# Kernel optimization log

Hardware: AMD Instinct MI355X
Metric: run time of the kernel (lower is better)

The kernel has to match this reference:

```python
import jax, jax.numpy as jnp
import numpy as np

EPS = 1e-5

def _ln(x, w, b):
    mu = jnp.mean(x, -1, keepdims=True)
    var = jnp.mean((x - mu) ** 2, -1, keepdims=True)
    return (x - mu) * jax.lax.rsqrt(var + EPS) * w + b

def setup_inputs() -> dict:
    key = jax.random.key(0)
    ks = jax.random.split(key, 12)
    B, H, W, C = 4, 32, 32, 768
    nh, hd, hidden = 12, 64, 3072
    s = lambda k, sh, fan: jax.random.normal(k, sh, jnp.float32) * (fan ** -0.5)
    return {
        "x": jax.random.normal(ks[0], (B, H, W, C), jnp.float32),
        "norm1_w": jnp.ones((C,), jnp.float32),
        "norm1_b": jnp.zeros((C,), jnp.float32),
        "qkv_w": s(ks[1], (C, 3 * C), C),
        "qkv_b": jnp.zeros((3 * C,), jnp.float32),
        "proj_w": s(ks[2], (C, C), C),
        "proj_b": jnp.zeros((C,), jnp.float32),
        "rel_h": jnp.ones((2 * H - 1, hd), jnp.float32),
        "rel_w": jnp.ones((2 * W - 1, hd), jnp.float32),
        "norm2_w": jnp.ones((C,), jnp.float32),
        "norm2_b": jnp.zeros((C,), jnp.float32),
        "mlp_w1": s(ks[3], (C, hidden), C),
        "mlp_b1": jnp.zeros((hidden,), jnp.float32),
        "mlp_w2": s(ks[4], (hidden, C), hidden),
        "mlp_b2": jnp.zeros((C,), jnp.float32),
    }

def reference(x, norm1_w, norm1_b, qkv_w, qkv_b, proj_w, proj_b, rel_h, rel_w,
              norm2_w, norm2_b, mlp_w1, mlp_b1, mlp_w2, mlp_b2):
    B, H, W, C = x.shape
    nh = 12
    hd = C // nh
    scale = hd ** -0.5
    S = H * W

    xn = _ln(x, norm1_w, norm1_b)
    qkv = (xn.reshape(B, S, C) @ qkv_w + qkv_b)            # [B,S,3C]
    qkv = qkv.reshape(B, S, 3, nh, hd).transpose(2, 0, 3, 1, 4).reshape(3, B * nh, S, hd)
    q, k, v = qkv[0], qkv[1], qkv[2]                        # [B*nh,S,hd]

    attn = jnp.einsum('bqd,bkd->bqk', q * scale, k)         # [B*nh,S,S]

    # relative position bias (q_size == k_size == H or W)
    idx_h = jnp.arange(H)[:, None] - jnp.arange(H)[None, :] + (H - 1)
    idx_w = jnp.arange(W)[:, None] - jnp.arange(W)[None, :] + (W - 1)
    Rh = rel_h[idx_h]                                       # [H,H,hd]
    Rw = rel_w[idx_w]                                       # [W,W,hd]
    q4 = q.reshape(B * nh, H, W, hd)                        # unscaled q, as in source
    bias_h = jnp.einsum('bhwc,hkc->bhwk', q4, Rh)           # [B*nh,H,W,H]
    bias_w = jnp.einsum('bhwc,wkc->bhwk', q4, Rw)           # [B*nh,H,W,W]
    attn = (attn.reshape(B * nh, H, W, H, W)
            + bias_h[:, :, :, :, None]
            + bias_w[:, :, :, None, :]).reshape(B * nh, S, S)

    attn = jax.nn.softmax(attn, axis=-1)
    out = jnp.einsum('bqk,bkd->bqd', attn, v)               # [B*nh,S,hd]
    out = out.reshape(B, nh, H, W, hd).transpose(0, 2, 3, 1, 4).reshape(B, H, W, C)
    x = out @ proj_w + proj_b + x

    xn = _ln(x, norm2_w, norm2_b)
    h = jax.nn.gelu(xn @ mlp_w1 + mlp_b1, approximate=False)
    return h @ mlp_w2 + mlp_b2 + x
```

## Files before the change

### kernel.cpp

```cpp
#include <hip/hip_runtime.h>
#include <hip/hip_bf16.h>
#include <cstdint>
#include <cstddef>

typedef __bf16 bf16x8 __attribute__((ext_vector_type(8)));
typedef float  f32x4  __attribute__((ext_vector_type(4)));
typedef unsigned short u16x8 __attribute__((ext_vector_type(8)));

#define S_TOT 1024
#define NH 12
#define HD 64
#define NBH 48
#define CDIM 768
#define L2E 1.44269504088896f

static __device__ __forceinline__ unsigned short f2bf(float f) {
    unsigned int u = __builtin_bit_cast(unsigned int, f);
    u += 0x7FFFu + ((u >> 16) & 1u);
    return (unsigned short)(u >> 16);
}

static __device__ __forceinline__ float exp2_raw(float x) {
    float r;
    asm("v_exp_f32 %0, %1" : "=v"(r) : "v"(x));
    return r;
}

static __device__ __forceinline__ float gelu_fast(float x) {
    float u = x * (1.0f + 0.044715f * x * x);
    float e = exp2_raw(-2.3022090f * u);
    return x / (1.0f + e);
}

static __device__ __forceinline__ void async16(void* lds, const void* g) {
    __builtin_amdgcn_global_load_lds(
        (const __attribute__((address_space(1))) unsigned int*)g,
        (__attribute__((address_space(3))) unsigned int*)lds, 16, 0, 0);
}

static __device__ __forceinline__ int xcd_swz(int orig, int nwg) {
    return (orig & 7) * (nwg >> 3) + (orig >> 3);
}

__launch_bounds__(256)
__global__ void ln_kernel(const float* __restrict__ x, const float* __restrict__ w,
                          const float* __restrict__ b, unsigned short* __restrict__ out)
{
    const int row = blockIdx.x;
    const int tid = threadIdx.x;
    const float* xr = x + (size_t)row * CDIM;
    float v0 = xr[tid], v1 = xr[tid + 256], v2 = xr[tid + 512];
    float s  = v0 + v1 + v2;
    float s2 = v0 * v0 + v1 * v1 + v2 * v2;
    #pragma unroll
    for (int off = 32; off > 0; off >>= 1) {
        s  += __shfl_xor(s,  off);
        s2 += __shfl_xor(s2, off);
    }
    __shared__ float ss[4], ss2[4];
    const int wid = tid >> 6;
    if ((tid & 63) == 0) { ss[wid] = s; ss2[wid] = s2; }
    __syncthreads();
    s  = ss[0] + ss[1] + ss[2] + ss[3];
    s2 = ss2[0] + ss2[1] + ss2[2] + ss2[3];
    const float mu  = s * (1.0f / CDIM);
    const float var = s2 * (1.0f / CDIM) - mu * mu;
    const float rs  = rsqrtf(var + 1e-5f);
    unsigned short* orow = out + (size_t)row * CDIM;
    float vv[3] = {v0, v1, v2};
    #pragma unroll
    for (int i = 0; i < 3; ++i) {
        int c = tid + i * 256;
        orow[c] = f2bf((vv[i] - mu) * rs * w[c] + b[c]);
    }
}

__launch_bounds__(256)
__global__ void wt_all_kernel(const float* __restrict__ qkv_w, const float* __restrict__ proj_w,
                              const float* __restrict__ w1, const float* __restrict__ w2,
                              unsigned short* __restrict__ wTq, unsigned short* __restrict__ wTp,
                              unsigned short* __restrict__ wT1, unsigned short* __restrict__ wT2)
{
    __shared__ float tile[32][33];
    int id = blockIdx.x;
    const float* W; unsigned short* WT; int K, N, ko, no;
    if (id < 1728)      { W = qkv_w;  WT = wTq; K = 768;  N = 2304;            ko = id % 24; no = id / 24; }
    else if (id < 2304) { W = proj_w; WT = wTp; K = 768;  N = 768;  id -= 1728; ko = id % 24; no = id / 24; }
    else if (id < 4608) { W = w1;     WT = wT1; K = 768;  N = 3072; id -= 2304; ko = id % 24; no = id / 24; }
    else                { W = w2;     WT = wT2; K = 3072; N = 768;  id -= 4608; ko = id % 96; no = id / 96; }
    const int k0 = ko * 32, n0 = no * 32;
    const int tx = threadIdx.x & 31, ty = threadIdx.x >> 5;
    #pragma unroll
    for (int i = 0; i < 4; ++i) {
        int kk = ty + i * 8;
        tile[kk][tx] = W[(size_t)(k0 + kk) * N + n0 + tx];
    }
    __syncthreads();
    #pragma unroll
    for (int i = 0; i < 4; ++i) {
        int nn = ty + i * 8;
        WT[(size_t)(n0 + nn) * K + k0 + tx] = f2bf(tile[tx][nn]);
    }
}

__launch_bounds__(256)
__global__ void vtrans_kernel(const unsigned short* __restrict__ v,
                              unsigned short* __restrict__ vT)
{
    __shared__ unsigned short tile[64][65];
    const int bh = blockIdx.x;
    const int s0 = blockIdx.y * 64;
    const int tid = threadIdx.x;
    #pragma unroll
    for (int it = 0; it < 2; ++it) {
        int idx = tid + it * 256;
        int r = idx >> 3, c0 = (idx & 7) * 8;
        *(u16x8*)&tile[r][c0] = *(const u16x8*)&v[((size_t)bh * S_TOT + s0 + r) * HD + c0];
    }
    __syncthreads();
    #pragma unroll
    for (int it = 0; it < 2; ++it) {
        int idx = tid + it * 256;
        int d = idx >> 3, sc = (idx & 7) * 8;
        u16x8 o;
        #pragma unroll
        for (int e = 0; e < 8; ++e) o[e] = tile[sc + e][d];
        *(u16x8*)&vT[((size_t)bh * HD + d) * S_TOT + s0 + sc] = o;
    }
}

template<int EPI>
__launch_bounds__(256)
__global__ void gemm64x128_kernel(const unsigned short* __restrict__ A,
                                  const unsigned short* __restrict__ BT,
                                  const float* __restrict__ bias,
                                  unsigned short* __restrict__ outh,
                                  int M, int N, int K)
{
    __shared__ __align__(16) unsigned short As[64 * 64];
    __shared__ __align__(16) unsigned short Bs[128 * 64];
    const int tid  = threadIdx.x;
    const int nwgx = gridDim.x;
    const int wg   = xcd_swz(blockIdx.y * nwgx + blockIdx.x, nwgx * gridDim.y);
    const int bm   = (wg % nwgx) * 64;
    const int bn   = (wg / nwgx) * 128;
    const int wid  = tid >> 6, lane = tid & 63;
    const int wr   = (wid >> 1) * 32, wc = (wid & 1) * 64;
    const int fr   = lane & 15, fk = lane >> 4;

    f32x4 acc[2][4] = {};

    for (int kk = 0; kk < K; kk += 64) {
        __syncthreads();
        #pragma unroll
        for (int it = 0; it < 4; ++it) {
            int idx = tid + it * 256;
            int r = idx >> 3;
            int j = (idx & 7) ^ (r & 7);
            async16(&Bs[idx * 8], &BT[(size_t)(bn + r) * K + kk + j * 8]);
            if (it < 2)
                async16(&As[idx * 8], &A[(size_t)(bm + r) * K + kk + j * 8]);
        }
        __syncthreads();
        #pragma unroll
        for (int ks = 0; ks < 2; ++ks) {
            bf16x8 af[2], bfv[4];
            #pragma unroll
            for (int i = 0; i < 2; ++i) {
                int Ra = wr + i * 16 + fr;
                af[i] = *(const bf16x8*)&As[Ra * 64 + (((ks * 4 + fk) ^ (Ra & 7)) * 8)];
            }
            #pragma unroll
            for (int j = 0; j < 4; ++j) {
                int Rb = wc + j * 16 + fr;
                bfv[j] = *(const bf16x8*)&Bs[Rb * 64 + (((ks * 4 + fk) ^ (Rb & 7)) * 8)];
            }
            __builtin_amdgcn_s_setprio(1);
            #pragma unroll
            for (int i = 0; i < 2; ++i)
                #pragma unroll
                for (int j = 0; j < 4; ++j)
                    acc[i][j] = __builtin_amdgcn_mfma_f32_16x16x32_bf16(af[i], bfv[j], acc[i][j], 0, 0, 0);
            __builtin_amdgcn_s_setprio(0);
        }
    }

    const int er = (lane >> 4) * 4;
    const int ec = lane & 15;
    #pragma unroll
    for (int i = 0; i < 2; ++i) {
        const int rowb = bm + wr + i * 16 + er;
        #pragma unroll
        for (int j = 0; j < 4; ++j) {
            const int col = bn + wc + j * 16 + ec;
            #pragma unroll
            for (int r = 0; r < 4; ++r) {
                const int row = rowb + r;
                float val = acc[i][j][r] + bias[col];
                if constexpr (EPI == 0) {
                    int bb = row >> 10, s = row & 1023;
                    int t  = col / CDIM;
                    int rem = col - t * CDIM;
                    int hh = rem >> 6, d = rem & 63;
                    outh[((size_t)(t * NBH + bb * NH + hh) * S_TOT + s) * HD + d] = f2bf(val);
                } else {
                    outh[(size_t)row * N + col] = f2bf(gelu_fast(val));
                }
            }
        }
    }
}

__launch_bounds__(256)
__global__ void gemm64_kernel(const unsigned short* __restrict__ A,
                              const unsigned short* __restrict__ BT,
                              const float* __restrict__ bias,
                              const float* __restrict__ res,
                              float* __restrict__ outf,
                              int M, int N, int K)
{
    __shared__ __align__(16) unsigned short As[64 * 64];
    __shared__ __align__(16) unsigned short Bs[64 * 64];
    const int tid  = threadIdx.x;
    const int nwgx = gridDim.x;
    const int wg   = xcd_swz(blockIdx.y * nwgx + blockIdx.x, nwgx * gridDim.y);
    const int bm   = (wg % nwgx) * 64;
    const int bn   = (wg / nwgx) * 64;
    const int wid  = tid >> 6, lane = tid & 63;
    const int wr   = (wid >> 1) * 32, wc = (wid & 1) * 32;
    const int fr   = lane & 15, fk = lane >> 4;

    f32x4 acc[2][2] = {};

    for (int kk = 0; kk < K; kk += 64) {
        __syncthreads();
        #pragma unroll
        for (int it = 0; it < 2; ++it) {
            int idx = tid + it * 256;
            int r = idx >> 3;
            int j = (idx & 7) ^ (r & 7);
            async16(&As[idx * 8], &A[(size_t)(bm + r) * K + kk + j * 8]);
            async16(&Bs[idx * 8], &BT[(size_t)(bn + r) * K + kk + j * 8]);
        }
        __syncthreads();
        #pragma unroll
        for (int ks = 0; ks < 2; ++ks) {
            bf16x8 af[2], bfv[2];
            #pragma unroll
            for (int i = 0; i < 2; ++i) {
                int Ra = wr + i * 16 + fr;
                af[i]  = *(const bf16x8*)&As[Ra * 64 + (((ks * 4 + fk) ^ (Ra & 7)) * 8)];
                int Rb = wc + i * 16 + fr;
                bfv[i] = *(const bf16x8*)&Bs[Rb * 64 + (((ks * 4 + fk) ^ (Rb & 7)) * 8)];
            }
            __builtin_amdgcn_s_setprio(1);
            #pragma unroll
            for (int i = 0; i < 2; ++i)
                #pragma unroll
                for (int j = 0; j < 2; ++j)
                    acc[i][j] = __builtin_amdgcn_mfma_f32_16x16x32_bf16(af[i], bfv[j], acc[i][j], 0, 0, 0);
            __builtin_amdgcn_s_setprio(0);
        }
    }

    const int er = (lane >> 4) * 4;
    const int ec = lane & 15;
    #pragma unroll
    for (int i = 0; i < 2; ++i) {
        const int rowb = bm + wr + i * 16 + er;
        #pragma unroll
        for (int j = 0; j < 2; ++j) {
            const int col = bn + wc + j * 16 + ec;
            #pragma unroll
            for (int r = 0; r < 4; ++r) {
                const int row = rowb + r;
                size_t idx = (size_t)row * N + col;
                outf[idx] = acc[i][j][r] + bias[col] + res[idx];
            }
        }
    }
}

__launch_bounds__(256)
__global__ void bias_kernel(const unsigned short* __restrict__ q,
                            const float* __restrict__ rel_h,
                            const float* __restrict__ rel_w,
                            float* __restrict__ biasH,
                            float* __restrict__ biasW)
{
    __shared__ __align__(16) unsigned short Bl[32 * 72];
    const int tid  = threadIdx.x;
    const int wid  = tid >> 6, lane = tid & 63;
    const int fr   = lane & 15, fk = lane >> 4;
    const int mt   = blockIdx.x;
    const int qc   = blockIdx.y;
    const int mode = blockIdx.z;
    const float* rel = mode ? rel_w : rel_h;
    float* outp = mode ? biasW : biasH;

    {
        int row = tid >> 3, c0 = (tid & 7) * 8;
        const float* rp = rel + (size_t)(qc + 31 - row) * HD + c0;
        u16x8 o;
        #pragma unroll
        for (int e = 0; e < 8; ++e) o[e] = f2bf(rp[e]);
        *(u16x8*)&Bl[row * 72 + c0] = o;
    }
    __syncthreads();

    const int ri = wid * 16 + fr;
    const int bh = mt * 2 + (ri >> 5);
    const int inner = ri & 31;
    const int s = mode ? (inner * 32 + qc) : (qc * 32 + inner);
    const unsigned short* arow = q + ((size_t)bh * S_TOT + s) * HD;

    f32x4 acc[2] = {};
    #pragma unroll
    for (int ks = 0; ks < 2; ++ks) {
        bf16x8 af = *(const bf16x8*)&arow[ks * 32 + fk * 8];
        #pragma unroll
        for (int nt = 0; nt < 2; ++nt) {
            bf16x8 bfv = *(const bf16x8*)&Bl[(nt * 16 + fr) * 72 + ks * 32 + fk * 8];
            acc[nt] = __builtin_amdgcn_mfma_f32_16x16x32_bf16(af, bfv, acc[nt], 0, 0, 0);
        }
    }

    const int g = lane >> 4, c = lane & 15;
    #pragma unroll
    for (int reg = 0; reg < 4; ++reg) {
        int ro = wid * 16 + g * 4 + reg;
        int bho = mt * 2 + (ro >> 5);
        int io  = ro & 31;
        int so  = mode ? (io * 32 + qc) : (qc * 32 + io);
        float* op = outp + ((size_t)bho * S_TOT + so) * 32;
        op[c]      = acc[0][reg] * L2E;
        op[16 + c] = acc[1][reg] * L2E;
    }
}

__launch_bounds__(256, 4)
__global__ void attn_kernel(const unsigned short* __restrict__ qkv,
                            const unsigned short* __restrict__ vT,
                            const float* __restrict__ biasH,
                            const float* __restrict__ biasW,
                            unsigned short* __restrict__ out)
{
    __shared__ __align__(16) unsigned short Ks[64 * 64];
    __shared__ __align__(16) unsigned short Vt[64 * 64];
    __shared__ __align__(16) unsigned short Pst[4][16][72];

    const int tid  = threadIdx.x;
    const int wid  = tid >> 6;
    const int lane = tid & 63;
    const int fr   = lane & 15, fk = lane >> 4;
    const int er   = (lane >> 4) * 4, ec = lane & 15;
    const int bh_  = blockIdx.x % NBH;
    const int qt   = blockIdx.x / NBH;
    const int row0 = qt * 64;
    const int b    = bh_ / NH, h = bh_ - b * NH;

    const unsigned short* q = qkv;
    const unsigned short* k = qkv + (size_t)NBH * S_TOT * HD;
    const size_t headoff  = (size_t)bh_ * S_TOT * HD;
    const size_t vheadoff = (size_t)bh_ * HD * S_TOT;

    #pragma unroll
    for (int it = 0; it < 2; ++it) {
        int idx = tid + it * 256;
        int r = idx >> 3;
        int j = (idx & 7) ^ (r & 7);
        async16(&Ks[idx * 8], &q[headoff + (size_t)(row0 + r) * HD + j * 8]);
    }
    __syncthreads();

    bf16x8 qf[2];
    {
        int Rq = wid * 16 + fr;
        qf[0] = *(const bf16x8*)&Ks[Rq * 64 + ((fk ^ (Rq & 7)) * 8)];
        qf[1] = *(const bf16x8*)&Ks[Rq * 64 + (((4 + fk) ^ (Rq & 7)) * 8)];
    }

    float bh0[4], bh1[4], bw0[4], bw1[4];
    {
        const int g = lane >> 4, c = lane & 15;
        #pragma unroll
        for (int reg = 0; reg < 4; ++reg) {
            int rt = row0 + wid * 16 + g * 4 + reg;
            const float* ph = biasH + ((size_t)bh_ * S_TOT + rt) * 32;
            const float* pw = biasW + ((size_t)bh_ * S_TOT + rt) * 32;
            bh0[reg] = ph[c];  bh1[reg] = ph[16 + c];
            bw0[reg] = pw[c];  bw1[reg] = pw[16 + c];
        }
    }

    const u16x8 ones_u = {0x3F80, 0x3F80, 0x3F80, 0x3F80, 0x3F80, 0x3F80, 0x3F80, 0x3F80};
    const bf16x8 ones = __builtin_bit_cast(bf16x8, ones_u);
    const float SCL = 0.125f * L2E;

    float m[4], l[4];
    f32x4 oacc[4];
    #pragma unroll
    for (int r = 0; r < 4; ++r) {
        m[r] = -1e30f; l[r] = 0.f;
        oacc[r][0] = 0.f; oacc[r][1] = 0.f; oacc[r][2] = 0.f; oacc[r][3] = 0.f;
    }

    for (int kt = 0; kt < 16; ++kt) {
        __syncthreads();
        #pragma unroll
        for (int it = 0; it < 2; ++it) {
            int idx = tid + it * 256;
            int r = idx >> 3;
            int j = (idx & 7) ^ (r & 7);
            async16(&Ks[idx * 8], &k[headoff + (size_t)(kt * 64 + r) * HD + j * 8]);
            async16(&Vt[idx * 8], &vT[vheadoff + (size_t)r * S_TOT + kt * 64 + j * 8]);
        }
        __syncthreads();

        f32x4 sacc[4] = {};
        __builtin_amdgcn_s_setprio(1);
        #pragma unroll
        for (int nt = 0; nt < 4; ++nt) {
            int Rk = nt * 16 + fr;
            bf16x8 b0 = *(const bf16x8*)&Ks[Rk * 64 + ((fk ^ (Rk & 7)) * 8)];
            bf16x8 b1 = *(const bf16x8*)&Ks[Rk * 64 + (((4 + fk) ^ (Rk & 7)) * 8)];
            sacc[nt] = __builtin_amdgcn_mfma_f32_16x16x32_bf16(qf[0], b0, sacc[nt], 0, 0, 0);
            sacc[nt] = __builtin_amdgcn_mfma_f32_16x16x32_bf16(qf[1], b1, sacc[nt], 0, 0, 0);
        }
        __builtin_amdgcn_s_setprio(0);

        float bhv[2][4];
        #pragma unroll
        for (int j = 0; j < 2; ++j) {
            int kh = kt * 2 + j;
            int src = ((lane >> 4) << 4) + (kh & 15);
            #pragma unroll
            for (int reg = 0; reg < 4; ++reg)
                bhv[j][reg] = (kh < 16) ? __shfl(bh0[reg], src) : __shfl(bh1[reg], src);
        }

        float tmax[4] = {-1e30f, -1e30f, -1e30f, -1e30f};
        #pragma unroll
        for (int nt = 0; nt < 4; ++nt) {
            #pragma unroll
            for (int reg = 0; reg < 4; ++reg) {
                float s_ = sacc[nt][reg] * SCL + bhv[nt >> 1][reg]
                         + ((nt & 1) ? bw1[reg] : bw0[reg]);
                sacc[nt][reg] = s_;
                tmax[reg] = fmaxf(tmax[reg], s_);
            }
        }
        #pragma unroll
        for (int reg = 0; reg < 4; ++reg) {
            #pragma unroll
            for (int off = 8; off > 0; off >>= 1)
                tmax[reg] = fmaxf(tmax[reg], __shfl_xor(tmax[reg], off));
            float mnew = fmaxf(m[reg], tmax[reg]);
            float c = exp2_raw(m[reg] - mnew);
            m[reg] = mnew;
            #pragma unroll
            for (int nt = 0; nt < 4; ++nt) {
                float p = exp2_raw(sacc[nt][reg] - mnew);
                Pst[wid][er + reg][nt * 16 + ec] = f2bf(p);
            }
            l[reg] *= c;
            #pragma unroll
            for (int nt = 0; nt < 4; ++nt) oacc[nt][reg] *= c;
        }

        __builtin_amdgcn_s_setprio(1);
        bf16x8 pa0 = *(const bf16x8*)&Pst[wid][fr][fk * 8];
        bf16x8 pa1 = *(const bf16x8*)&Pst[wid][fr][32 + fk * 8];
        f32x4 ps = {};
        ps = __builtin_amdgcn_mfma_f32_16x16x32_bf16(pa0, ones, ps, 0, 0, 0);
        ps = __builtin_amdgcn_mfma_f32_16x16x32_bf16(pa1, ones, ps, 0, 0, 0);
        #pragma unroll
        for (int nt = 0; nt < 4; ++nt) {
            int Rv = nt * 16 + fr;
            bf16x8 vb0 = *(const bf16x8*)&Vt[Rv * 64 + ((fk ^ (Rv & 7)) * 8)];
            bf16x8 vb1 = *(const bf16x8*)&Vt[Rv * 64 + (((4 + fk) ^ (Rv & 7)) * 8)];
            oacc[nt] = __builtin_amdgcn_mfma_f32_16x16x32_bf16(pa0, vb0, oacc[nt], 0, 0, 0);
            oacc[nt] = __builtin_amdgcn_mfma_f32_16x16x32_bf16(pa1, vb1, oacc[nt], 0, 0, 0);
        }
        __builtin_amdgcn_s_setprio(0);
        #pragma unroll
        for (int reg = 0; reg < 4; ++reg) l[reg] += ps[reg];
    }

    #pragma unroll
    for (int reg = 0; reg < 4; ++reg) {
        float inv = 1.0f / l[reg];
        int srow = row0 + wid * 16 + er + reg;
        #pragma unroll
        for (int nt = 0; nt < 4; ++nt) {
            out[((size_t)(b * S_TOT + srow)) * CDIM + h * HD + nt * 16 + ec] =
                f2bf(oacc[nt][reg] * inv);
        }
    }
}

extern "C" void kernel_launch(void* const* d_in, const int* in_sizes, int n_in,
                              void* d_out, int out_size, void* d_ws, size_t ws_size,
                              hipStream_t stream)
{
    const float* x      = (const float*)d_in[0];
    const float* n1w    = (const float*)d_in[1];
    const float* n1b    = (const float*)d_in[2];
    const float* qkv_w  = (const float*)d_in[3];
    const float* qkv_b  = (const float*)d_in[4];
    const float* proj_w = (const float*)d_in[5];
    const float* proj_b = (const float*)d_in[6];
    const float* rel_h  = (const float*)d_in[7];
    const float* rel_w  = (const float*)d_in[8];
    const float* n2w    = (const float*)d_in[9];
    const float* n2b    = (const float*)d_in[10];
    const float* w1     = (const float*)d_in[11];
    const float* b1     = (const float*)d_in[12];
    const float* w2     = (const float*)d_in[13];
    const float* b2     = (const float*)d_in[14];

    char* ws = (char*)d_ws;
    unsigned short* qkvbf = (unsigned short*)(ws + 0);
    float*          biasH = (float*)(ws + 18874368);
    float*          biasW = (float*)(ws + 25165824);
    unsigned short* hbf   = (unsigned short*)(ws + 0);
    float*          x1    = (float*)(ws + 25165824);
    unsigned short* xnbf  = (unsigned short*)(ws + 37748736);
    unsigned short* vTbuf = (unsigned short*)(ws + 37748736);
    unsigned short* wTq   = (unsigned short*)(ws + 44040192);
    unsigned short* wTp   = (unsigned short*)(ws + 47579136);
    unsigned short* wT1   = (unsigned short*)(ws + 48758784);
    unsigned short* wT2   = (unsigned short*)(ws + 53477376);
    unsigned short* aout  = (unsigned short*)(ws + 58195968);

    wt_all_kernel<<<6912, 256, 0, stream>>>(qkv_w, proj_w, w1, w2, wTq, wTp, wT1, wT2);

    ln_kernel<<<4096, 256, 0, stream>>>(x, n1w, n1b, xnbf);
    gemm64x128_kernel<0><<<dim3(64, 18), 256, 0, stream>>>(xnbf, wTq, qkv_b, qkvbf, 4096, 2304, 768);
    vtrans_kernel<<<dim3(48, 16), 256, 0, stream>>>(qkvbf + (size_t)2 * NBH * S_TOT * HD, vTbuf);
    bias_kernel<<<dim3(24, 32, 2), 256, 0, stream>>>(qkvbf, rel_h, rel_w, biasH, biasW);
    attn_kernel<<<768, 256, 0, stream>>>(qkvbf, vTbuf, biasH, biasW, aout);
    gemm64_kernel<<<dim3(64, 12), 256, 0, stream>>>(aout, wTp, proj_b, x, x1, 4096, 768, 768);
    ln_kernel<<<4096, 256, 0, stream>>>(x1, n2w, n2b, xnbf);
    gemm64x128_kernel<2><<<dim3(64, 24), 256, 0, stream>>>(xnbf, wT1, b1, hbf, 4096, 3072, 768);
    gemm64_kernel<<<dim3(64, 12), 256, 0, stream>>>(hbf, wT2, b2, x1, (float*)d_out, 4096, 768, 3072);
}
```

Baseline: 188.2 us.

## Double-buffer LDS tiles in gemm64 and attention kernels with async prefetch

Both the 64x64 GEMM and the flash-attention kernel now keep two LDS buffers and issue the async global-to-LDS loads for tile t+1 before computing tile t. Each iteration waits only on the older loads with a partial vmcnt wait, then a barrier. The goal is to hide global load latency behind MFMA work instead of stalling on a full sync each iteration. LDS use doubles, and the attention kernel's launch bound drops from 4 to 3 blocks per CU, which may lower occupancy. The manual vmcnt counts also depend on the exact number of loads issued per thread.

Measured after the change: 188.8 us. About the same (+0.3%).

```diff
diff --git a/kernel.cpp b/kernel.cpp
--- a/kernel.cpp
+++ b/kernel.cpp
@@ -219,8 +219,8 @@
                               float* __restrict__ outf,
                               int M, int N, int K)
 {
-    __shared__ __align__(16) unsigned short As[64 * 64];
-    __shared__ __align__(16) unsigned short Bs[64 * 64];
+    __shared__ __align__(16) unsigned short As[2][64 * 64];
+    __shared__ __align__(16) unsigned short Bs[2][64 * 64];
     const int tid  = threadIdx.x;
     const int nwgx = gridDim.x;
     const int wg   = xcd_swz(blockIdx.y * nwgx + blockIdx.x, nwgx * gridDim.y);
@@ -231,27 +231,45 @@
     const int fr   = lane & 15, fk = lane >> 4;
 
     f32x4 acc[2][2] = {};
-
-    for (int kk = 0; kk < K; kk += 64) {
-        __syncthreads();
-        #pragma unroll
-        for (int it = 0; it < 2; ++it) {
-            int idx = tid + it * 256;
-            int r = idx >> 3;
-            int j = (idx & 7) ^ (r & 7);
-            async16(&As[idx * 8], &A[(size_t)(bm + r) * K + kk + j * 8]);
-            async16(&Bs[idx * 8], &BT[(size_t)(bn + r) * K + kk + j * 8]);
-        }
-        __syncthreads();
+    const int nt = K >> 6;
+
+    #pragma unroll
+    for (int it = 0; it < 2; ++it) {
+        int idx = tid + it * 256;
+        int r = idx >> 3;
+        int j = (idx & 7) ^ (r & 7);
+        async16(&As[0][idx * 8], &A[(size_t)(bm + r) * K + j * 8]);
+        async16(&Bs[0][idx * 8], &BT[(size_t)(bn + r) * K + j * 8]);
+    }
+
+    int cur = 0;
+    for (int t = 0; t < nt; ++t) {
+        if (t + 1 < nt) {
+            const int kk = (t + 1) << 6;
+            #pragma unroll
+            for (int it = 0; it < 2; ++it) {
+                int idx = tid + it * 256;
+                int r = idx >> 3;
+                int j = (idx & 7) ^ (r & 7);
+                async16(&As[cur ^ 1][idx * 8], &A[(size_t)(bm + r) * K + kk + j * 8]);
+                async16(&Bs[cur ^ 1][idx * 8], &BT[(size_t)(bn + r) * K + kk + j * 8]);
+            }
+            asm volatile("s_waitcnt vmcnt(4)" ::: "memory");
+        } else {
+            asm volatile("s_waitcnt vmcnt(0)" ::: "memory");
+        }
+        __builtin_amdgcn_s_barrier();
+        const unsigned short* Ac = As[cur];
+        const unsigned short* Bc = Bs[cur];
         #pragma unroll
         for (int ks = 0; ks < 2; ++ks) {
             bf16x8 af[2], bfv[2];
             #pragma unroll
             for (int i = 0; i < 2; ++i) {
                 int Ra = wr + i * 16 + fr;
-                af[i]  = *(const bf16x8*)&As[Ra * 64 + (((ks * 4 + fk) ^ (Ra & 7)) * 8)];
+                af[i]  = *(const bf16x8*)&Ac[Ra * 64 + (((ks * 4 + fk) ^ (Ra & 7)) * 8)];
                 int Rb = wc + i * 16 + fr;
-                bfv[i] = *(const bf16x8*)&Bs[Rb * 64 + (((ks * 4 + fk) ^ (Rb & 7)) * 8)];
+                bfv[i] = *(const bf16x8*)&Bc[Rb * 64 + (((ks * 4 + fk) ^ (Rb & 7)) * 8)];
             }
             __builtin_amdgcn_s_setprio(1);
             #pragma unroll
@@ -261,6 +279,8 @@
                     acc[i][j] = __builtin_amdgcn_mfma_f32_16x16x32_bf16(af[i], bfv[j], acc[i][j], 0, 0, 0);
             __builtin_amdgcn_s_setprio(0);
         }
+        __builtin_amdgcn_s_barrier();
+        cur ^= 1;
     }
 
     const int er = (lane >> 4) * 4;
@@ -338,15 +358,15 @@
     }
 }
 
-__launch_bounds__(256, 4)
+__launch_bounds__(256, 3)
 __global__ void attn_kernel(const unsigned short* __restrict__ qkv,
                             const unsigned short* __restrict__ vT,
                             const float* __restrict__ biasH,
                             const float* __restrict__ biasW,
                             unsigned short* __restrict__ out)
 {
-    __shared__ __align__(16) unsigned short Ks[64 * 64];
-    __shared__ __align__(16) unsigned short Vt[64 * 64];
+    __shared__ __align__(16) unsigned short Ks[2][64 * 64];
+    __shared__ __align__(16) unsigned short Vt[2][64 * 64];
     __shared__ __align__(16) unsigned short Pst[4][16][72];
 
     const int tid  = threadIdx.x;
@@ -369,15 +389,15 @@
         int idx = tid + it * 256;
         int r = idx >> 3;
         int j = (idx & 7) ^ (r & 7);
-        async16(&Ks[idx * 8], &q[headoff + (size_t)(row0 + r) * HD + j * 8]);
+        async16(&Ks[0][idx * 8], &q[headoff + (size_t)(row0 + r) * HD + j * 8]);
     }
     __syncthreads();
 
     bf16x8 qf[2];
     {
         int Rq = wid * 16 + fr;
-        qf[0] = *(const bf16x8*)&Ks[Rq * 64 + ((fk ^ (Rq & 7)) * 8)];
-        qf[1] = *(const bf16x8*)&Ks[Rq * 64 + (((4 + fk) ^ (Rq & 7)) * 8)];
+        qf[0] = *(const bf16x8*)&Ks[0][Rq * 64 + ((fk ^ (Rq & 7)) * 8)];
+        qf[1] = *(const bf16x8*)&Ks[0][Rq * 64 + (((4 + fk) ^ (Rq & 7)) * 8)];
     }
 
     float bh0[4], bh1[4], bw0[4], bw1[4];
@@ -392,6 +412,16 @@
             bw0[reg] = pw[c];  bw1[reg] = pw[16 + c];
         }
     }
+    __syncthreads();
+
+    #pragma unroll
+    for (int it = 0; it < 2; ++it) {
+        int idx = tid + it * 256;
+        int r = idx >> 3;
+        int j = (idx & 7) ^ (r & 7);
+        async16(&Ks[0][idx * 8], &k[headoff + (size_t)r * HD + j * 8]);
+        async16(&Vt[0][idx * 8], &vT[vheadoff + (size_t)r * S_TOT + j * 8]);
+    }
 
     const u16x8 ones_u = {0x3F80, 0x3F80, 0x3F80, 0x3F80, 0x3F80, 0x3F80, 0x3F80, 0x3F80};
     const bf16x8 ones = __builtin_bit_cast(bf16x8, ones_u);
@@ -405,25 +435,34 @@
         oacc[r][0] = 0.f; oacc[r][1] = 0.f; oacc[r][2] = 0.f; oacc[r][3] = 0.f;
     }
 
+    int cur = 0;
     for (int kt = 0; kt < 16; ++kt) {
-        __syncthreads();
-        #pragma unroll
-        for (int it = 0; it < 2; ++it) {
-            int idx = tid + it * 256;
-            int r = idx >> 3;
-            int j = (idx & 7) ^ (r & 7);
-            async16(&Ks[idx * 8], &k[headoff + (size_t)(kt * 64 + r) * HD + j * 8]);
-            async16(&Vt[idx * 8], &vT[vheadoff + (size_t)r * S_TOT + kt * 64 + j * 8]);
-        }
-        __syncthreads();
+        if (kt + 1 < 16) {
+            #pragma unroll
+            for (int it = 0; it < 2; ++it) {
+                int idx = tid + it * 256;
+                int r = idx >> 3;
+                int j = (idx & 7) ^ (r & 7);
+                async16(&Ks[cur ^ 1][idx * 8],
+                        &k[headoff + (size_t)((kt + 1) * 64 + r) * HD + j * 8]);
+                async16(&Vt[cur ^ 1][idx * 8],
+                        &vT[vheadoff + (size_t)r * S_TOT + (kt + 1) * 64 + j * 8]);
+            }
+            asm volatile("s_waitcnt vmcnt(4)" ::: "memory");
+        } else {
+            asm volatile("s_waitcnt vmcnt(0)" ::: "memory");
+        }
+        __builtin_amdgcn_s_barrier();
+        const unsigned short* Kc = Ks[cur];
+        const unsigned short* Vc = Vt[cur];
 
         f32x4 sacc[4] = {};
         __builtin_amdgcn_s_setprio(1);
         #pragma unroll
         for (int nt = 0; nt < 4; ++nt) {
             int Rk = nt * 16 + fr;
-            bf16x8 b0 = *(const bf16x8*)&Ks[Rk * 64 + ((fk ^ (Rk & 7)) * 8)];
-            bf16x8 b1 = *(const bf16x8*)&Ks[Rk * 64 + (((4 + fk) ^ (Rk & 7)) * 8)];
+            bf16x8 b0 = *(const bf16x8*)&Kc[Rk * 64 + ((fk ^ (Rk & 7)) * 8)];
+            bf16x8 b1 = *(const bf16x8*)&Kc[Rk * 64 + (((4 + fk) ^ (Rk & 7)) * 8)];
             sacc[nt] = __builtin_amdgcn_mfma_f32_16x16x32_bf16(qf[0], b0, sacc[nt], 0, 0, 0);
             sacc[nt] = __builtin_amdgcn_mfma_f32_16x16x32_bf16(qf[1], b1, sacc[nt], 0, 0, 0);
         }
@@ -477,14 +516,17 @@
         #pragma unroll
         for (int nt = 0; nt < 4; ++nt) {
             int Rv = nt * 16 + fr;
-            bf16x8 vb0 = *(const bf16x8*)&Vt[Rv * 64 + ((fk ^ (Rv & 7)) * 8)];
-            bf16x8 vb1 = *(const bf16x8*)&Vt[Rv * 64 + (((4 + fk) ^ (Rv & 7)) * 8)];
+            bf16x8 vb0 = *(const bf16x8*)&Vc[Rv * 64 + ((fk ^ (Rv & 7)) * 8)];
+            bf16x8 vb1 = *(const bf16x8*)&Vc[Rv * 64 + (((4 + fk) ^ (Rv & 7)) * 8)];
             oacc[nt] = __builtin_amdgcn_mfma_f32_16x16x32_bf16(pa0, vb0, oacc[nt], 0, 0, 0);
             oacc[nt] = __builtin_amdgcn_mfma_f32_16x16x32_bf16(pa1, vb1, oacc[nt], 0, 0, 0);
         }
         __builtin_amdgcn_s_setprio(0);
         #pragma unroll
         for (int reg = 0; reg < 4; ++reg) l[reg] += ps[reg];
+
+        __builtin_amdgcn_s_barrier();
+        cur ^= 1;
     }
 
     #pragma unroll
```

## Double-buffer LDS tiles in gemm64 kernel to overlap loads with MFMA

Applied to the files above, without the earlier changes.

Converts the 64x64 GEMM (the projection and MLP-down path with residual) to a two-stage LDS ping-pong. The next K-tile is prefetched asynchronously while the current one is consumed, with explicit vmcnt waits and raw barriers in place of the two syncthreads per iteration. This is meant to hide global-to-LDS latency behind the MFMA work. In exchange, LDS per block doubles, which may lower occupancy, and correctness now depends on the manual waitcnt counting being right.

Result: no change. 187.5 us (-0.4%).

```diff
diff --git a/kernel.cpp b/kernel.cpp
--- a/kernel.cpp
+++ b/kernel.cpp
@@ -219,8 +219,8 @@
                               float* __restrict__ outf,
                               int M, int N, int K)
 {
-    __shared__ __align__(16) unsigned short As[64 * 64];
-    __shared__ __align__(16) unsigned short Bs[64 * 64];
+    __shared__ __align__(16) unsigned short As[2][64 * 64];
+    __shared__ __align__(16) unsigned short Bs[2][64 * 64];
     const int tid  = threadIdx.x;
     const int nwgx = gridDim.x;
     const int wg   = xcd_swz(blockIdx.y * nwgx + blockIdx.x, nwgx * gridDim.y);
@@ -231,27 +231,45 @@
     const int fr   = lane & 15, fk = lane >> 4;
 
     f32x4 acc[2][2] = {};
-
-    for (int kk = 0; kk < K; kk += 64) {
-        __syncthreads();
-        #pragma unroll
-        for (int it = 0; it < 2; ++it) {
-            int idx = tid + it * 256;
-            int r = idx >> 3;
-            int j = (idx & 7) ^ (r & 7);
-            async16(&As[idx * 8], &A[(size_t)(bm + r) * K + kk + j * 8]);
-            async16(&Bs[idx * 8], &BT[(size_t)(bn + r) * K + kk + j * 8]);
-        }
-        __syncthreads();
+    const int nt = K >> 6;
+
+    #pragma unroll
+    for (int it = 0; it < 2; ++it) {
+        int idx = tid + it * 256;
+        int r = idx >> 3;
+        int j = (idx & 7) ^ (r & 7);
+        async16(&As[0][idx * 8], &A[(size_t)(bm + r) * K + j * 8]);
+        async16(&Bs[0][idx * 8], &BT[(size_t)(bn + r) * K + j * 8]);
+    }
+
+    int cur = 0;
+    for (int t = 0; t < nt; ++t) {
+        if (t + 1 < nt) {
+            const int kk = (t + 1) << 6;
+            #pragma unroll
+            for (int it = 0; it < 2; ++it) {
+                int idx = tid + it * 256;
+                int r = idx >> 3;
+                int j = (idx & 7) ^ (r & 7);
+                async16(&As[cur ^ 1][idx * 8], &A[(size_t)(bm + r) * K + kk + j * 8]);
+                async16(&Bs[cur ^ 1][idx * 8], &BT[(size_t)(bn + r) * K + kk + j * 8]);
+            }
+            asm volatile("s_waitcnt vmcnt(4)" ::: "memory");
+        } else {
+            asm volatile("s_waitcnt vmcnt(0)" ::: "memory");
+        }
+        __builtin_amdgcn_s_barrier();
+        const unsigned short* Ac = As[cur];
+        const unsigned short* Bc = Bs[cur];
         #pragma unroll
         for (int ks = 0; ks < 2; ++ks) {
             bf16x8 af[2], bfv[2];
             #pragma unroll
             for (int i = 0; i < 2; ++i) {
                 int Ra = wr + i * 16 + fr;
-                af[i]  = *(const bf16x8*)&As[Ra * 64 + (((ks * 4 + fk) ^ (Ra & 7)) * 8)];
+                af[i]  = *(const bf16x8*)&Ac[Ra * 64 + (((ks * 4 + fk) ^ (Ra & 7)) * 8)];
                 int Rb = wc + i * 16 + fr;
-                bfv[i] = *(const bf16x8*)&Bs[Rb * 64 + (((ks * 4 + fk) ^ (Rb & 7)) * 8)];
+                bfv[i] = *(const bf16x8*)&Bc[Rb * 64 + (((ks * 4 + fk) ^ (Rb & 7)) * 8)];
             }
             __builtin_amdgcn_s_setprio(1);
             #pragma unroll
@@ -261,6 +279,8 @@
                     acc[i][j] = __builtin_amdgcn_mfma_f32_16x16x32_bf16(af[i], bfv[j], acc[i][j], 0, 0, 0);
             __builtin_amdgcn_s_setprio(0);
         }
+        __builtin_amdgcn_s_barrier();
+        cur ^= 1;
     }
 
     const int er = (lane >> 4) * 4;
```
